# Performance work log

Measured on AMD Instinct MI355X. Metric: run time of the kernel, lower is better.

The kernel has to match this reference:

```python
import jax, jax.numpy as jnp
import numpy as np


def setup_inputs() -> dict:
    key = jax.random.key(0)
    ks = jax.random.split(key, 6)
    B, M, H = 256, 64, 512
    memory_state = jax.random.normal(ks[0], (B, M, M, M), dtype=jnp.float32) * 0.02
    hidden_state = jax.random.normal(ks[1], (B, H), dtype=jnp.float32)
    role1 = jnp.tanh(jax.random.normal(ks[2], (B, M), dtype=jnp.float32))
    role2 = jnp.tanh(jax.random.normal(ks[3], (B, M), dtype=jnp.float32))
    filer = jnp.tanh(jax.random.normal(ks[4], (B, M), dtype=jnp.float32))
    W_gate = jax.random.normal(ks[5], (1, H), dtype=jnp.float32) * (1.0 / np.sqrt(H))
    b_gate = jnp.zeros((1,), dtype=jnp.float32)
    return {"memory_state": memory_state, "hidden_state": hidden_state,
            "role1": role1, "role2": role2, "filer": filer,
            "W_gate": W_gate, "b_gate": b_gate}


def reference(memory_state, hidden_state, role1, role2, filer, W_gate, b_gate):
    M = memory_state.shape[1]
    # write gate: sigmoid(Linear(h) + 1), shape [B, 1]
    write_gate = jax.nn.sigmoid(hidden_state @ W_gate.T + b_gate + 1.0)
    # outer product of roles: [B, M, M]
    role = jnp.einsum('br,bt->brt', role1, role2)
    # read from 3D associative memory: [B, M]
    prev_info = jnp.einsum('brt,brtf->bf', role, memory_state)
    cur_info = write_gate * (filer - prev_info)
    scale = 1.0 / M
    # gated outer-product write
    new_memory = memory_state + jnp.einsum('brt,bf->brtf', role, cur_info * scale)
    # norm-clip rescale
    mem_norm = jnp.linalg.norm(new_memory.reshape(new_memory.shape[0], -1), axis=-1)
    mem_norm = jax.nn.relu(mem_norm - 1.0) + 1.0
    new_memory = new_memory / mem_norm[:, None, None, None]
    return new_memory
```

## Files before the change

### kernel.cpp

```cpp
#include <hip/hip_runtime.h>
#include <math.h>

#define M 64
#define B 256
#define T 256

typedef float f32x4 __attribute__((ext_vector_type(4)));

__device__ __forceinline__ float wave_sum64(float v) {
    #pragma unroll
    for (int m = 32; m >= 1; m >>= 1) v += __shfl_xor(v, m);
    return v;
}

__global__ __launch_bounds__(T) void k_reduce(
    const float* __restrict__ mem, const float* __restrict__ role1,
    const float* __restrict__ role2, float* __restrict__ prev_part,
    float* __restrict__ ss_part)
{
    const int b   = blockIdx.x >> 3;
    const int sp  = blockIdx.x & 7;
    const int tid = threadIdx.x;

    __shared__ float  role_s[512];
    __shared__ float4 part[4][16];
    __shared__ float  ss_lds[4];

    for (int i = tid; i < 512; i += T) {
        const int rt = sp * 512 + i;
        role_s[i] = role1[b * M + (rt >> 6)] * role2[b * M + (rt & 63)];
    }
    __syncthreads();

    const float4* mem4 = (const float4*)(mem + (size_t)b * 262144);
    const int f4 = tid & 15, rsub = tid >> 4;

    float4 ap = make_float4(0.f, 0.f, 0.f, 0.f);
    float  ss = 0.f;
    #pragma unroll 8
    for (int i = 0; i < 32; ++i) {
        const int lrt = rsub + i * 16;
        const float4 v = mem4[(sp * 512 + lrt) * 16 + f4];
        const float  r = role_s[lrt];
        ap.x = fmaf(r, v.x, ap.x);
        ap.y = fmaf(r, v.y, ap.y);
        ap.z = fmaf(r, v.z, ap.z);
        ap.w = fmaf(r, v.w, ap.w);
        ss = fmaf(v.x, v.x, ss);
        ss = fmaf(v.y, v.y, ss);
        ss = fmaf(v.z, v.z, ss);
        ss = fmaf(v.w, v.w, ss);
    }

    #pragma unroll
    for (int m = 16; m <= 32; m <<= 1) {
        ap.x += __shfl_xor(ap.x, m);
        ap.y += __shfl_xor(ap.y, m);
        ap.z += __shfl_xor(ap.z, m);
        ap.w += __shfl_xor(ap.w, m);
    }
    const float ssw = wave_sum64(ss);

    const int wave = tid >> 6, lane = tid & 63;
    if (lane < 16) part[wave][lane] = ap;
    if (lane == 0) ss_lds[wave] = ssw;
    __syncthreads();

    if (tid < 16) {
        float4 a0 = part[0][tid], a1 = part[1][tid], a2 = part[2][tid], a3 = part[3][tid];
        float4 s;
        s.x = (a0.x + a1.x) + (a2.x + a3.x);
        s.y = (a0.y + a1.y) + (a2.y + a3.y);
        s.z = (a0.z + a1.z) + (a2.z + a3.z);
        s.w = (a0.w + a1.w) + (a2.w + a3.w);
        ((float4*)prev_part)[(size_t)(b * 8 + sp) * 16 + tid] = s;
    }
    if (tid == 0)
        ss_part[b * 8 + sp] = (ss_lds[0] + ss_lds[1]) + (ss_lds[2] + ss_lds[3]);
}

__global__ __launch_bounds__(T) void k_write(
    const float* __restrict__ mem, const float* __restrict__ hidden,
    const float* __restrict__ role1, const float* __restrict__ role2,
    const float* __restrict__ filer, const float* __restrict__ W_gate,
    const float* __restrict__ b_gate, const float* __restrict__ prev_part,
    const float* __restrict__ ss_part, float* __restrict__ out)
{
    const int b   = blockIdx.x >> 3;
    const int sp  = blockIdx.x & 7;
    const int tid = threadIdx.x;

    __shared__ float role_s[512];
    __shared__ float c2_s[M];
    __shared__ float inv_s;

    if (tid < M) {
        const int f = tid;
        float p = 0.f;
        #pragma unroll
        for (int s = 0; s < 8; ++s) p += prev_part[(size_t)(b * 8 + s) * M + f];
        float ssm = 0.f;
        #pragma unroll
        for (int s = 0; s < 8; ++s) ssm += ss_part[b * 8 + s];

        float g = 0.f;
        #pragma unroll
        for (int j = 0; j < 8; ++j)
            g = fmaf(hidden[(size_t)b * 512 + f + j * 64], W_gate[f + j * 64], g);
        g = wave_sum64(g);
        g = 1.f / (1.f + expf(-(g + b_gate[0] + 1.f)));

        const float fil = filer[b * M + f];
        const float cur = g * (fil - p);
        const float d1   = wave_sum64(p * cur);
        const float ssc  = wave_sum64(cur * cur);
        const float r1   = role1[b * M + f];
        const float r2   = role2[b * M + f];
        const float ssr1 = wave_sum64(r1 * r1);
        const float ssr2 = wave_sum64(r2 * r2);

        const float sc = 1.0f / (float)M;
        const float ns = ssm + 2.f * sc * d1 + sc * sc * ssr1 * ssr2 * ssc;
        const float inv = 1.0f / fmaxf(sqrtf(ns), 1.0f);
        c2_s[f] = cur * sc * inv;
        if (f == 0) inv_s = inv;
    }
    for (int i = tid; i < 512; i += T) {
        const int rt = sp * 512 + i;
        role_s[i] = role1[b * M + (rt >> 6)] * role2[b * M + (rt & 63)];
    }
    __syncthreads();

    const float  inv = inv_s;
    const float4 c   = ((const float4*)c2_s)[tid & 15];
    const float4* mem4 = (const float4*)(mem + (size_t)b * 262144);
    f32x4* out4 = (f32x4*)(out + (size_t)b * 262144);
    const int f4 = tid & 15, rsub = tid >> 4;

    #pragma unroll 8
    for (int i = 0; i < 32; ++i) {
        const int lrt = rsub + i * 16;
        const int idx = (sp * 512 + lrt) * 16 + f4;
        const float4 v = mem4[idx];
        const float  r = role_s[lrt];
        f32x4 o;
        o.x = fmaf(r, c.x, v.x * inv);
        o.y = fmaf(r, c.y, v.y * inv);
        o.z = fmaf(r, c.z, v.z * inv);
        o.w = fmaf(r, c.w, v.w * inv);
        __builtin_nontemporal_store(o, &out4[idx]);
    }
}

extern "C" void kernel_launch(void* const* d_in, const int* in_sizes, int n_in,
                              void* d_out, int out_size, void* d_ws, size_t ws_size,
                              hipStream_t stream) {
    const float* mem    = (const float*)d_in[0];
    const float* hidden = (const float*)d_in[1];
    const float* role1  = (const float*)d_in[2];
    const float* role2  = (const float*)d_in[3];
    const float* filer  = (const float*)d_in[4];
    const float* Wg     = (const float*)d_in[5];
    const float* bg     = (const float*)d_in[6];
    float* out = (float*)d_out;

    float* ws        = (float*)d_ws;
    float* prev_part = ws;
    float* ss_part   = ws + 131072;

    hipLaunchKernelGGL(k_reduce, dim3(B * 8), dim3(T), 0, stream,
                       mem, role1, role2, prev_part, ss_part);
    hipLaunchKernelGGL(k_write, dim3(B * 8), dim3(T), 0, stream,
                       mem, hidden, role1, role2, filer, Wg, bg,
                       prev_part, ss_part, out);
}
```

Measured before the change: 131.4 us.

## Fuse reduce and write kernels with per-batch atomic barrier

Merges the reduction and write passes into one kernel, where the 8 blocks of each batch synchronise through an atomic counter before computing the gate and norm and writing output. Each block rereads its memory slice right after reducing it, aiming for cache hits instead of a second HBM pass, and one kernel launch is removed. It relies on all 8 blocks of a batch being co-resident and adds a memset plus spin-waiting.

```diff
diff --git a/kernel.cpp b/kernel.cpp
--- a/kernel.cpp
+++ b/kernel.cpp
@@ -13,10 +13,13 @@
     return v;
 }
 
-__global__ __launch_bounds__(T) void k_reduce(
-    const float* __restrict__ mem, const float* __restrict__ role1,
-    const float* __restrict__ role2, float* __restrict__ prev_part,
-    float* __restrict__ ss_part)
+__global__ __launch_bounds__(T) void k_all(
+    const float* __restrict__ mem, const float* __restrict__ hidden,
+    const float* __restrict__ role1, const float* __restrict__ role2,
+    const float* __restrict__ filer, const float* __restrict__ W_gate,
+    const float* __restrict__ b_gate, float* __restrict__ prev_part,
+    float* __restrict__ ss_part, int* __restrict__ cnt,
+    float* __restrict__ out)
 {
     const int b   = blockIdx.x >> 3;
     const int sp  = blockIdx.x & 7;
@@ -25,6 +28,8 @@
     __shared__ float  role_s[512];
     __shared__ float4 part[4][16];
     __shared__ float  ss_lds[4];
+    __shared__ float  c2_s[M];
+    __shared__ float  inv_s;
 
     for (int i = tid; i < 512; i += T) {
         const int rt = sp * 512 + i;
@@ -77,22 +82,17 @@
     }
     if (tid == 0)
         ss_part[b * 8 + sp] = (ss_lds[0] + ss_lds[1]) + (ss_lds[2] + ss_lds[3]);
-}
+    __syncthreads();
 
-__global__ __launch_bounds__(T) void k_write(
-    const float* __restrict__ mem, const float* __restrict__ hidden,
-    const float* __restrict__ role1, const float* __restrict__ role2,
-    const float* __restrict__ filer, const float* __restrict__ W_gate,
-    const float* __restrict__ b_gate, const float* __restrict__ prev_part,
-    const float* __restrict__ ss_part, float* __restrict__ out)
-{
-    const int b   = blockIdx.x >> 3;
-    const int sp  = blockIdx.x & 7;
-    const int tid = threadIdx.x;
-
-    __shared__ float role_s[512];
-    __shared__ float c2_s[M];
-    __shared__ float inv_s;
+    if (tid == 0) {
+        __hip_atomic_fetch_add(&cnt[b], 1, __ATOMIC_RELEASE,
+                               __HIP_MEMORY_SCOPE_AGENT);
+        while (__hip_atomic_load(&cnt[b], __ATOMIC_ACQUIRE,
+                                 __HIP_MEMORY_SCOPE_AGENT) < 8)
+            __builtin_amdgcn_s_sleep(1);
+    }
+    __syncthreads();
+    __threadfence();
 
     if (tid < M) {
         const int f = tid;
@@ -125,18 +125,11 @@
         c2_s[f] = cur * sc * inv;
         if (f == 0) inv_s = inv;
     }
-    for (int i = tid; i < 512; i += T) {
-        const int rt = sp * 512 + i;
-        role_s[i] = role1[b * M + (rt >> 6)] * role2[b * M + (rt & 63)];
-    }
     __syncthreads();
 
     const float  inv = inv_s;
-    const float4 c   = ((const float4*)c2_s)[tid & 15];
-    const float4* mem4 = (const float4*)(mem + (size_t)b * 262144);
+    const float4 c   = ((const float4*)c2_s)[f4];
     f32x4* out4 = (f32x4*)(out + (size_t)b * 262144);
-    const int f4 = tid & 15, rsub = tid >> 4;
-
     #pragma unroll 8
     for (int i = 0; i < 32; ++i) {
         const int lrt = rsub + i * 16;
@@ -167,10 +160,10 @@
     float* ws        = (float*)d_ws;
     float* prev_part = ws;
     float* ss_part   = ws + 131072;
+    int*   cnt       = (int*)(ws + 133120);
 
-    hipLaunchKernelGGL(k_reduce, dim3(B * 8), dim3(T), 0, stream,
-                       mem, role1, role2, prev_part, ss_part);
-    hipLaunchKernelGGL(k_write, dim3(B * 8), dim3(T), 0, stream,
+    hipMemsetAsync(cnt, 0, B * sizeof(int), stream);
+    hipLaunchKernelGGL(k_all, dim3(B * 8), dim3(T), 0, stream,
                        mem, hidden, role1, role2, filer, Wg, bg,
-                       prev_part, ss_part, out);
+                       prev_part, ss_part, cnt, out);
 }
```

New measurement: 327.2 us. 2.49x slower.
